# Kernel optimization log

Measured on AMD Instinct MI355X. Metric: run time of the kernel, lower is better.

The kernel has to match this reference:

```python
import jax, jax.numpy as jnp
import numpy as np

B = 65536          # batch
E = 512            # embedding_dim
SL = 128           # speed_latent_dim
H = 256            # hidden_size
NB = 6             # num_branch
D = E + SL         # 640, branch input dim


def _linear_init(k, din, dout):
    bound = 1.0 / np.sqrt(din)
    kw, kb = jax.random.split(k)
    W = jax.random.uniform(kw, (din, dout), minval=-bound, maxval=bound, dtype=jnp.float32)
    b = jax.random.uniform(kb, (dout,), minval=-bound, maxval=bound, dtype=jnp.float32)
    return W, b


def setup_inputs() -> dict:
    key = jax.random.key(0)
    ks = jax.random.split(key, 10)
    embedding = jax.random.normal(ks[0], (B, E), dtype=jnp.float32)
    speed = jax.random.uniform(ks[1], (B, 1), dtype=jnp.float32)
    command = jax.random.randint(ks[2], (B,), 1, NB + 1)  # values in 1..6

    # speed_in: Linear(1,H) -> ReLU -> Linear(H,SL)
    si_W1, si_b1 = _linear_init(ks[3], 1, H)
    si_W2, si_b2 = _linear_init(ks[4], H, SL)

    # speed_out: Linear(D,H) -> ReLU -> Linear(H,H) -> ReLU -> Linear(H,1)
    so_W1, so_b1 = _linear_init(ks[5], D, H)
    so_W2, so_b2 = _linear_init(ks[6], H, H)
    so_W3, so_b3 = _linear_init(ks[7], H, 1)

    # NB branches, each Linear(D,H)->ReLU->Linear(H,H)->ReLU->Linear(H,3)->Sigmoid
    def mk_branch(k):
        k1, k2, k3 = jax.random.split(k, 3)
        W1, b1 = _linear_init(k1, D, H)
        W2, b2 = _linear_init(k2, H, H)
        W3, b3 = _linear_init(k3, H, 3)
        return W1, b1, W2, b2, W3, b3

    bW1, bb1, bW2, bb2, bW3, bb3 = jax.vmap(mk_branch)(jax.random.split(ks[8], NB))

    return {
        "embedding": embedding, "speed": speed, "command": command,
        "si_W1": si_W1, "si_b1": si_b1, "si_W2": si_W2, "si_b2": si_b2,
        "bW1": bW1, "bb1": bb1, "bW2": bW2, "bb2": bb2, "bW3": bW3, "bb3": bb3,
        "so_W1": so_W1, "so_b1": so_b1, "so_W2": so_W2, "so_b2": so_b2,
        "so_W3": so_W3, "so_b3": so_b3,
    }


def reference(embedding, speed, command,
              si_W1, si_b1, si_W2, si_b2,
              bW1, bb1, bW2, bb2, bW3, bb3,
              so_W1, so_b1, so_W2, so_b2, so_W3, so_b3):
    # speed_in MLP and concat
    s = jax.nn.relu(speed @ si_W1 + si_b1) @ si_W2 + si_b2          # [B, SL]
    emb = jnp.concatenate([embedding, s], axis=1)                    # [B, D]

    # all branches computed densely (as in the torch module), then one-hot mask
    h1 = jax.nn.relu(jnp.einsum('bd,ndh->nbh', emb, bW1) + bb1[:, None, :])   # [NB,B,H]
    h2 = jax.nn.relu(jnp.einsum('nbh,nhk->nbk', h1, bW2) + bb2[:, None, :])   # [NB,B,H]
    out = jax.nn.sigmoid(jnp.einsum('nbk,nko->nbo', h2, bW3) + bb3[:, None, :])  # [NB,B,3]

    mask = (jnp.arange(NB)[:, None] == (command - 1)[None, :]).astype(out.dtype)  # [NB,B]
    control_pred = jnp.sum(out * mask[:, :, None], axis=0)           # [B, 3]

    # speed prediction head
    sp = jax.nn.relu(emb @ so_W1 + so_b1)
    sp = jax.nn.relu(sp @ so_W2 + so_b2)
    speed_pred = sp @ so_W3 + so_b3                                  # [B, 1]

    return control_pred, speed_pred
```

## Files before the change

### kernel.cpp

```cpp
#include <hip/hip_runtime.h>
#include <cstdint>
#include <cstddef>

typedef _Float16 f16;
typedef f16 f16x8 __attribute__((ext_vector_type(8)));
typedef float f32x4 __attribute__((ext_vector_type(4)));

#define B_ROWS 65536
#define TILE_M 128
#define NT_BRANCH 518
#define NT_SPEED 512

constexpr size_t OFF_SF16   = 0;
constexpr size_t SZ_SF16    = (size_t)B_ROWS * 128 * 2;
constexpr size_t OFF_SIW2T  = OFF_SF16 + SZ_SF16;
constexpr size_t SZ_SIW2T   = (size_t)128 * 256 * 2;
constexpr size_t OFF_BW1T   = OFF_SIW2T + SZ_SIW2T;
constexpr size_t SZ_BW1T    = (size_t)6 * 256 * 640 * 2;
constexpr size_t OFF_BW2T   = OFF_BW1T + SZ_BW1T;
constexpr size_t SZ_BW2T    = (size_t)6 * 256 * 256 * 2;
constexpr size_t OFF_SOW1T  = OFF_BW2T + SZ_BW2T;
constexpr size_t SZ_SOW1T   = (size_t)256 * 640 * 2;
constexpr size_t OFF_SOW2T  = OFF_SOW1T + SZ_SOW1T;
constexpr size_t SZ_SOW2T   = (size_t)256 * 256 * 2;
constexpr size_t OFF_BW3T16 = OFF_SOW2T + SZ_SOW2T;
constexpr size_t SZ_BW3T16  = (size_t)6 * 16 * 256 * 2;
constexpr size_t OFF_SOW3T16= OFF_BW3T16 + SZ_BW3T16;
constexpr size_t SZ_SOW3T16 = (size_t)16 * 256 * 2;
constexpr size_t OFF_COUNTS = OFF_SOW3T16 + SZ_SOW3T16;
constexpr size_t OFF_CURSORS= OFF_COUNTS + 256;
constexpr size_t OFF_BINBASE= OFF_CURSORS + 256;
constexpr size_t OFF_TILECMD= OFF_BINBASE + 256;
constexpr size_t OFF_PERM   = OFF_TILECMD + 4352;
constexpr size_t WS_NEEDED  = OFF_PERM + (size_t)NT_BRANCH * TILE_M * 4;

#define MFMA16(a, b, c) __builtin_amdgcn_mfma_f32_16x16x32_f16(a, b, c, 0, 0, 0)
#define BARSYNC() asm volatile("s_waitcnt lgkmcnt(0)\n\ts_barrier" ::: "memory")

__global__ void prep_kernel(const float* __restrict__ siW2,
                            const float* __restrict__ bW1,
                            const float* __restrict__ bW2,
                            const float* __restrict__ soW1,
                            const float* __restrict__ soW2,
                            const float* __restrict__ bW3,
                            const float* __restrict__ soW3,
                            f16* __restrict__ siW2T, f16* __restrict__ bW1T,
                            f16* __restrict__ bW2T, f16* __restrict__ soW1T,
                            f16* __restrict__ soW2T,
                            f16* __restrict__ bW3T16, f16* __restrict__ soW3T16,
                            int* __restrict__ counts, int* __restrict__ cursors,
                            int* __restrict__ perm)
{
    const int bx = blockIdx.x;
    const int tx = threadIdx.x, ty = threadIdx.y;
    const int tid = ty * 32 + tx;
    if (bx >= 1601) {
        const int ib = bx - 1601;
        const int idx = ib * 256 + tid;
        if (idx < NT_BRANCH * TILE_M) perm[idx] = -1;
        if (ib == 0 && tid < 6) { counts[tid] = 0; cursors[tid] = 0; }
        return;
    }
    if (bx == 1600) {
        for (int i = tid; i < 6 * 16 * 256; i += 256) {
            const int c = i >> 12, rem = i & 4095, n = rem >> 8, k = rem & 255;
            bW3T16[i] = (n < 3) ? (f16)bW3[((size_t)c * 256 + k) * 3 + n] : (f16)0;
        }
        for (int i = tid; i < 16 * 256; i += 256) {
            const int n = i >> 8, k = i & 255;
            soW3T16[i] = (n == 0) ? (f16)soW3[k] : (f16)0;
        }
        return;
    }
    const float* in; f16* out; int R, C, lb;
    if (bx < 960)       { int m = bx / 160;        lb = bx - m * 160;       in = bW1 + (size_t)m * 640 * 256; out = bW1T + (size_t)m * 640 * 256; R = 640; C = 256; }
    else if (bx < 1344) { int m = (bx - 960) / 64; lb = (bx - 960) - m * 64; in = bW2 + (size_t)m * 256 * 256; out = bW2T + (size_t)m * 256 * 256; R = 256; C = 256; }
    else if (bx < 1504) { lb = bx - 1344; in = soW1; out = soW1T; R = 640; C = 256; }
    else if (bx < 1568) { lb = bx - 1504; in = soW2; out = soW2T; R = 256; C = 256; }
    else                { lb = bx - 1568; in = siW2; out = siW2T; R = 256; C = 128; }
    const int txt = C >> 5;
    const int c0 = (lb % txt) << 5;
    const int r0 = (lb / txt) << 5;
    __shared__ float tile[32][33];
    #pragma unroll
    for (int i = 0; i < 4; ++i)
        tile[tx][ty + 8 * i] = in[(size_t)(r0 + ty + 8 * i) * C + c0 + tx];
    __syncthreads();
    #pragma unroll
    for (int i = 0; i < 4; ++i)
        out[(size_t)(c0 + ty + 8 * i) * R + r0 + tx] = (f16)tile[ty + 8 * i][tx];
}

__global__ __launch_bounds__(256) void speedin_kernel(
    const float* __restrict__ speed,
    const float* __restrict__ siW1, const float* __restrict__ sib1,
    const f16* __restrict__ siW2T, const float* __restrict__ sib2,
    const int* __restrict__ cmd,
    f16* __restrict__ sF16, int* __restrict__ counts)
{
    __shared__ f16 H[64 * 264];
    __shared__ float spd[64];
    __shared__ int h[6];
    const int tid = threadIdx.x;
    const int rb = blockIdx.x * 64;
    if (tid < 6) h[tid] = 0;
    __syncthreads();
    if (tid < 64) {
        spd[tid] = speed[rb + tid];
        atomicAdd(&h[cmd[rb + tid] - 1], 1);
    }
    __syncthreads();
    if (tid < 6 && h[tid] > 0) atomicAdd(&counts[tid], h[tid]);
    {
        const float w1 = siW1[tid], b1v = sib1[tid];
        #pragma unroll 4
        for (int r = 0; r < 64; ++r) {
            float hv = spd[r] * w1 + b1v;
            H[r * 264 + tid] = (f16)(hv > 0.f ? hv : 0.f);
        }
    }
    __syncthreads();
    const int w = tid >> 6, lane = tid & 63, lq = lane >> 4, l16 = lane & 15;
    const int nb = w * 32;
    f32x4 acc[4][2];
    #pragma unroll
    for (int mt = 0; mt < 4; ++mt)
        #pragma unroll
        for (int nt = 0; nt < 2; ++nt)
            acc[mt][nt] = (f32x4){0.f, 0.f, 0.f, 0.f};
    for (int ks = 0; ks < 8; ++ks) {
        const int koff = ks * 32 + lq * 8;
        f16x8 af[4], bf[2];
        #pragma unroll
        for (int mt = 0; mt < 4; ++mt)
            af[mt] = *(const f16x8*)(&H[(mt * 16 + l16) * 264 + koff]);
        #pragma unroll
        for (int nt = 0; nt < 2; ++nt)
            bf[nt] = *(const f16x8*)(siW2T + (size_t)(nb + nt * 16 + l16) * 256 + koff);
        #pragma unroll
        for (int mt = 0; mt < 4; ++mt)
            #pragma unroll
            for (int nt = 0; nt < 2; ++nt)
                acc[mt][nt] = MFMA16(af[mt], bf[nt], acc[mt][nt]);
    }
    #pragma unroll
    for (int mt = 0; mt < 4; ++mt)
        #pragma unroll
        for (int nt = 0; nt < 2; ++nt) {
            const int n = nb + nt * 16 + l16;
            const float bv = sib2[n];
            #pragma unroll
            for (int r2 = 0; r2 < 4; ++r2) {
                const int m = mt * 16 + lq * 4 + r2;
                sF16[(size_t)(rb + m) * 128 + n] = (f16)(acc[mt][nt][r2] + bv);
            }
        }
}

__global__ void plan_kernel(const int* __restrict__ counts,
                            int* __restrict__ binBase, int* __restrict__ tile_cmd) {
    __shared__ int tbase[7];
    if (threadIdx.x == 0) {
        int base = 0, tb = 0;
        for (int c = 0; c < 6; ++c) {
            binBase[c] = base;
            tbase[c] = tb;
            const int nt = (counts[c] + TILE_M - 1) >> 7;
            tb += nt;
            base += nt << 7;
        }
        tbase[6] = tb;
    }
    __syncthreads();
    for (int t = threadIdx.x; t < NT_BRANCH; t += 256) {
        int c = -1;
        #pragma unroll
        for (int j = 0; j < 6; ++j)
            if (t >= tbase[j] && t < tbase[j + 1]) c = j;
        tile_cmd[t] = c;
    }
}

__global__ void place_kernel(const int* __restrict__ cmd,
                             const int* __restrict__ binBase,
                             int* __restrict__ cursors, int* __restrict__ perm) {
    __shared__ int lcnt[6], lbase[6];
    const int tid = threadIdx.x;
    if (tid < 6) lcnt[tid] = 0;
    __syncthreads();
    const int i = blockIdx.x * 256 + tid;
    const int c = cmd[i] - 1;
    const int myr = atomicAdd(&lcnt[c], 1);
    __syncthreads();
    if (tid < 6) lbase[tid] = atomicAdd(&cursors[tid], lcnt[tid]);
    __syncthreads();
    perm[binBase[c] + lbase[c] + myr] = i;
}

__device__ __forceinline__ void stage_load2(const float* __restrict__ srcF,
                                            const f16* __restrict__ srcH,
                                            int kc, int p, f16x8* v) {
    if (kc < 8) {
        const float* s = srcF + kc * 64 + p * 16;
        const float4 f0 = ((const float4*)s)[0];
        const float4 f1 = ((const float4*)s)[1];
        const float4 f2 = ((const float4*)s)[2];
        const float4 f3 = ((const float4*)s)[3];
        f16x8 a, b;
        a[0] = (f16)f0.x; a[1] = (f16)f0.y; a[2] = (f16)f0.z; a[3] = (f16)f0.w;
        a[4] = (f16)f1.x; a[5] = (f16)f1.y; a[6] = (f16)f1.z; a[7] = (f16)f1.w;
        b[0] = (f16)f2.x; b[1] = (f16)f2.y; b[2] = (f16)f2.z; b[3] = (f16)f2.w;
        b[4] = (f16)f3.x; b[5] = (f16)f3.y; b[6] = (f16)f3.z; b[7] = (f16)f3.w;
        v[0] = a; v[1] = b;
    } else {
        const f16* s = srcH + (kc - 8) * 64 + p * 16;
        v[0] = ((const f16x8*)s)[0];
        v[1] = ((const f16x8*)s)[1];
    }
}

__global__ __launch_bounds__(512, 3) void heads_kernel(
    const float* __restrict__ emb,
    const f16* __restrict__ sF16,
    const int* __restrict__ perm, const int* __restrict__ tile_cmd,
    const f16* __restrict__ bW1T, const f16* __restrict__ bW2T,
    const f16* __restrict__ bW3T16,
    const float* __restrict__ bb1, const float* __restrict__ bb2,
    const float* __restrict__ bb3,
    const f16* __restrict__ soW1T, const f16* __restrict__ soW2T,
    const f16* __restrict__ soW3T16,
    const float* __restrict__ sob1, const float* __restrict__ sob2,
    const float* __restrict__ sob3,
    float* __restrict__ out)
{
    __shared__ f16 smem[33792];
    __shared__ int rowIdx[TILE_M];
    const int bx = blockIdx.x;
    const int tid = threadIdx.x;
    const bool is_speed = (bx >= NT_BRANCH);
    const f16 *W1T, *W2T, *W3T;
    const float *bias1, *bias2, *bias3;
    if (is_speed) {
        const int t = bx - NT_BRANCH;
        if (tid < TILE_M) rowIdx[tid] = t * TILE_M + tid;
        W1T = soW1T; W2T = soW2T; W3T = soW3T16;
        bias1 = sob1; bias2 = sob2; bias3 = sob3;
    } else {
        const int c = tile_cmd[bx];
        if (c < 0) return;
        if (tid < TILE_M) rowIdx[tid] = perm[bx * TILE_M + tid];
        W1T = bW1T + (size_t)c * 256 * 640;
        W2T = bW2T + (size_t)c * 256 * 256;
        W3T = bW3T16 + (size_t)c * 16 * 256;
        bias1 = bb1 + c * 256; bias2 = bb2 + c * 256; bias3 = bb3 + c * 3;
    }
    __syncthreads();

    const int r = tid >> 2, p = tid & 3;
    int growS = rowIdx[r]; if (growS < 0) growS = 0;
    const float* srcF = emb + (size_t)growS * 512;
    const f16*   srcH = sF16 + (size_t)growS * 128;
    const int pOff = r * 72 + p * 16;

    const int w = tid >> 6, lane = tid & 63, lq = lane >> 4, l16 = lane & 15;
    const int nb = w * 32;
    const f16* brow0 = W1T + (size_t)(nb + l16) * 640;
    const f16* brow1 = W1T + (size_t)(nb + 16 + l16) * 640;

    f32x4 acc[8][2];
    #pragma unroll
    for (int mt = 0; mt < 8; ++mt)
        #pragma unroll
        for (int nt = 0; nt < 2; ++nt)
            acc[mt][nt] = (f32x4){0.f, 0.f, 0.f, 0.f};

    f16x8 sreg[3][2];
    #pragma unroll
    for (int j = 0; j < 3; ++j)
        stage_load2(srcF, srcH, j, p, sreg[j]);
    f16x8 Bb[2][2];
    #pragma unroll
    for (int ks = 0; ks < 2; ++ks) {
        Bb[ks][0] = *(const f16x8*)(brow0 + ks * 32 + lq * 8);
        Bb[ks][1] = *(const f16x8*)(brow1 + ks * 32 + lq * 8);
    }
    *(f16x8*)(smem + pOff) = sreg[0][0];
    *(f16x8*)(smem + pOff + 8) = sreg[0][1];
    BARSYNC();

    #pragma unroll
    for (int kc = 0; kc < 10; ++kc) {
        const f16* cur = smem + (kc & 1) * 9216;
        if (kc < 9) {
            f16* dst = smem + ((kc + 1) & 1) * 9216 + pOff;
            *(f16x8*)(dst)     = sreg[(kc + 1) % 3][0];
            *(f16x8*)(dst + 8) = sreg[(kc + 1) % 3][1];
        }
        if (kc < 7)
            stage_load2(srcF, srcH, kc + 3, p, sreg[kc % 3]);
        f16x8 Bn[2][2];
        if (kc < 9) {
            #pragma unroll
            for (int ks = 0; ks < 2; ++ks) {
                Bn[ks][0] = *(const f16x8*)(brow0 + (kc + 1) * 64 + ks * 32 + lq * 8);
                Bn[ks][1] = *(const f16x8*)(brow1 + (kc + 1) * 64 + ks * 32 + lq * 8);
            }
        }
        #pragma unroll
        for (int ks = 0; ks < 2; ++ks)
            #pragma unroll
            for (int mh = 0; mh < 2; ++mh) {
                f16x8 a[4];
                #pragma unroll
                for (int mt = 0; mt < 4; ++mt)
                    a[mt] = *(const f16x8*)(cur + ((mh * 4 + mt) * 16 + l16) * 72 + ks * 32 + lq * 8);
                #pragma unroll
                for (int mt = 0; mt < 4; ++mt) {
                    acc[mh * 4 + mt][0] = MFMA16(a[mt], Bb[ks][0], acc[mh * 4 + mt][0]);
                    acc[mh * 4 + mt][1] = MFMA16(a[mt], Bb[ks][1], acc[mh * 4 + mt][1]);
                }
            }
        if (kc < 9) {
            #pragma unroll
            for (int ks = 0; ks < 2; ++ks)
                #pragma unroll
                for (int nt = 0; nt < 2; ++nt)
                    Bb[ks][nt] = Bn[ks][nt];
        }
        BARSYNC();
    }

    const f16* brow2[2];
    #pragma unroll
    for (int nt = 0; nt < 2; ++nt)
        brow2[nt] = W2T + (size_t)(nb + nt * 16 + l16) * 256;
    f16x8 Bd[2][2];
    #pragma unroll
    for (int nt = 0; nt < 2; ++nt)
        Bd[0][nt] = *(const f16x8*)(brow2[nt] + lq * 8);

    #pragma unroll
    for (int mt = 0; mt < 8; ++mt)
        #pragma unroll
        for (int nt = 0; nt < 2; ++nt) {
            const int n = nb + nt * 16 + l16;
            const float bv = bias1[n];
            #pragma unroll
            for (int r2 = 0; r2 < 4; ++r2) {
                const int m = mt * 16 + lq * 4 + r2;
                const float v = acc[mt][nt][r2] + bv;
                smem[m * 264 + n] = (f16)(v > 0.f ? v : 0.f);
            }
            acc[mt][nt] = (f32x4){0.f, 0.f, 0.f, 0.f};
        }
    BARSYNC();

    #pragma unroll
    for (int ks = 0; ks < 8; ++ks) {
        if (ks < 7) {
            #pragma unroll
            for (int nt = 0; nt < 2; ++nt)
                Bd[(ks + 1) & 1][nt] = *(const f16x8*)(brow2[nt] + (ks + 1) * 32 + lq * 8);
        }
        #pragma unroll
        for (int mh = 0; mh < 2; ++mh) {
            f16x8 a[4];
            #pragma unroll
            for (int mt = 0; mt < 4; ++mt)
                a[mt] = *(const f16x8*)(&smem[((mh * 4 + mt) * 16 + l16) * 264 + ks * 32 + lq * 8]);
            #pragma unroll
            for (int mt = 0; mt < 4; ++mt) {
                acc[mh * 4 + mt][0] = MFMA16(a[mt], Bd[ks & 1][0], acc[mh * 4 + mt][0]);
                acc[mh * 4 + mt][1] = MFMA16(a[mt], Bd[ks & 1][1], acc[mh * 4 + mt][1]);
            }
        }
    }
    BARSYNC();
    #pragma unroll
    for (int mt = 0; mt < 8; ++mt)
        #pragma unroll
        for (int nt = 0; nt < 2; ++nt) {
            const int n = nb + nt * 16 + l16;
            const float bv = bias2[n];
            #pragma unroll
            for (int r2 = 0; r2 < 4; ++r2) {
                const int m = mt * 16 + lq * 4 + r2;
                const float v = acc[mt][nt][r2] + bv;
                smem[m * 264 + n] = (f16)(v > 0.f ? v : 0.f);
            }
        }
    BARSYNC();
    {
        f32x4 acc3 = (f32x4){0.f, 0.f, 0.f, 0.f};
        const f16* w3row = W3T + (size_t)l16 * 256;
        #pragma unroll
        for (int ks = 0; ks < 8; ++ks) {
            const int koff = ks * 32 + lq * 8;
            const f16x8 af = *(const f16x8*)(&smem[(w * 16 + l16) * 264 + koff]);
            const f16x8 bf = *(const f16x8*)(w3row + koff);
            acc3 = MFMA16(af, bf, acc3);
        }
        const int orow = w * 16 + lq * 4;
        if (!is_speed) {
            if (l16 < 3) {
                const float b3 = bias3[l16];
                #pragma unroll
                for (int r2 = 0; r2 < 4; ++r2) {
                    const int g = rowIdx[orow + r2];
                    if (g >= 0)
                        out[(size_t)g * 3 + l16] = 1.f / (1.f + __expf(-(acc3[r2] + b3)));
                }
            }
        } else {
            if (l16 == 0) {
                const float b3 = bias3[0];
                #pragma unroll
                for (int r2 = 0; r2 < 4; ++r2) {
                    const int g = rowIdx[orow + r2];
                    if (g >= 0)
                        out[(size_t)3 * B_ROWS + g] = acc3[r2] + b3;
                }
            }
        }
    }
}

extern "C" void kernel_launch(void* const* d_in, const int* in_sizes, int n_in,
                              void* d_out, int out_size, void* d_ws, size_t ws_size,
                              hipStream_t stream) {
    (void)in_sizes; (void)n_in; (void)out_size; (void)ws_size;
    const float* embedding = (const float*)d_in[0];
    const float* speed     = (const float*)d_in[1];
    const int*   command   = (const int*)d_in[2];
    const float* si_W1 = (const float*)d_in[3];
    const float* si_b1 = (const float*)d_in[4];
    const float* si_W2 = (const float*)d_in[5];
    const float* si_b2 = (const float*)d_in[6];
    const float* bW1   = (const float*)d_in[7];
    const float* bb1   = (const float*)d_in[8];
    const float* bW2   = (const float*)d_in[9];
    const float* bb2   = (const float*)d_in[10];
    const float* bW3   = (const float*)d_in[11];
    const float* bb3   = (const float*)d_in[12];
    const float* so_W1 = (const float*)d_in[13];
    const float* so_b1 = (const float*)d_in[14];
    const float* so_W2 = (const float*)d_in[15];
    const float* so_b2 = (const float*)d_in[16];
    const float* so_W3 = (const float*)d_in[17];
    const float* so_b3 = (const float*)d_in[18];
    float* out = (float*)d_out;

    char* ws = (char*)d_ws;
    f16* sF16   = (f16*)(ws + OFF_SF16);
    f16* siW2T  = (f16*)(ws + OFF_SIW2T);
    f16* bW1T   = (f16*)(ws + OFF_BW1T);
    f16* bW2T   = (f16*)(ws + OFF_BW2T);
    f16* soW1T  = (f16*)(ws + OFF_SOW1T);
    f16* soW2T  = (f16*)(ws + OFF_SOW2T);
    f16* bW3T16 = (f16*)(ws + OFF_BW3T16);
    f16* soW3T16= (f16*)(ws + OFF_SOW3T16);
    int* counts = (int*)(ws + OFF_COUNTS);
    int* cursors= (int*)(ws + OFF_CURSORS);
    int* binBase= (int*)(ws + OFF_BINBASE);
    int* tile_cmd = (int*)(ws + OFF_TILECMD);
    int* perm   = (int*)(ws + OFF_PERM);

    prep_kernel<<<1860, dim3(32, 8), 0, stream>>>(
        si_W2, bW1, bW2, so_W1, so_W2, bW3, so_W3,
        siW2T, bW1T, bW2T, soW1T, soW2T, bW3T16, soW3T16,
        counts, cursors, perm);
    speedin_kernel<<<1024, 256, 0, stream>>>(
        speed, si_W1, si_b1, siW2T, si_b2, command, sF16, counts);
    plan_kernel<<<1, 256, 0, stream>>>(counts, binBase, tile_cmd);
    place_kernel<<<256, 256, 0, stream>>>(command, binBase, cursors, perm);
    heads_kernel<<<NT_BRANCH + NT_SPEED, 512, 0, stream>>>(
        embedding, sF16, perm, tile_cmd,
        bW1T, bW2T, bW3T16, bb1, bb2, bb3,
        soW1T, soW2T, soW3T16, so_b1, so_b2, so_b3, out);
}
```

Before: 366.0 us.

## Pre-convert embedding to fp16 concatenated activation buffer in speedin kernel

The speedin kernel now converts the fp32 embedding to fp16 and writes it, together with the speed latent, into a single row-major [B,640] fp16 buffer. The heads kernel reads its A operand only from this buffer with uniform 16-byte loads and a 4-deep register prefetch, instead of loading and converting fp32 rows. Each embedding row is gathered by one branch tile and one speed tile, so the conversion cost and fp32 read traffic in the heads kernel drop. The cost is an extra 80MB fp16 write plus re-read through a larger workspace.

```diff
diff --git a/kernel.cpp b/kernel.cpp
--- a/kernel.cpp
+++ b/kernel.cpp
@@ -11,9 +11,9 @@
 #define NT_BRANCH 518
 #define NT_SPEED 512
 
-constexpr size_t OFF_SF16   = 0;
-constexpr size_t SZ_SF16    = (size_t)B_ROWS * 128 * 2;
-constexpr size_t OFF_SIW2T  = OFF_SF16 + SZ_SF16;
+constexpr size_t OFF_AF16   = 0;
+constexpr size_t SZ_AF16    = (size_t)B_ROWS * 640 * 2;
+constexpr size_t OFF_SIW2T  = OFF_AF16 + SZ_AF16;
 constexpr size_t SZ_SIW2T   = (size_t)128 * 256 * 2;
 constexpr size_t OFF_BW1T   = OFF_SIW2T + SZ_SIW2T;
 constexpr size_t SZ_BW1T    = (size_t)6 * 256 * 640 * 2;
@@ -92,11 +92,12 @@
 }
 
 __global__ __launch_bounds__(256) void speedin_kernel(
+    const float* __restrict__ emb,
     const float* __restrict__ speed,
     const float* __restrict__ siW1, const float* __restrict__ sib1,
     const f16* __restrict__ siW2T, const float* __restrict__ sib2,
     const int* __restrict__ cmd,
-    f16* __restrict__ sF16, int* __restrict__ counts)
+    f16* __restrict__ AF16, int* __restrict__ counts)
 {
     __shared__ f16 H[64 * 264];
     __shared__ float spd[64];
@@ -112,6 +113,20 @@
     __syncthreads();
     if (tid < 6 && h[tid] > 0) atomicAdd(&counts[tid], h[tid]);
     {
+        const int rr = tid >> 2, pp = tid & 3;
+        const float* src = emb + (size_t)(rb + rr) * 512 + pp * 128;
+        f16* dst = AF16 + (size_t)(rb + rr) * 640 + pp * 128;
+        #pragma unroll 4
+        for (int i = 0; i < 16; ++i) {
+            const float4 f0 = ((const float4*)src)[2 * i];
+            const float4 f1 = ((const float4*)src)[2 * i + 1];
+            f16x8 v;
+            v[0] = (f16)f0.x; v[1] = (f16)f0.y; v[2] = (f16)f0.z; v[3] = (f16)f0.w;
+            v[4] = (f16)f1.x; v[5] = (f16)f1.y; v[6] = (f16)f1.z; v[7] = (f16)f1.w;
+            *(f16x8*)(dst + i * 8) = v;
+        }
+    }
+    {
         const float w1 = siW1[tid], b1v = sib1[tid];
         #pragma unroll 4
         for (int r = 0; r < 64; ++r) {
@@ -152,7 +167,7 @@
             #pragma unroll
             for (int r2 = 0; r2 < 4; ++r2) {
                 const int m = mt * 16 + lq * 4 + r2;
-                sF16[(size_t)(rb + m) * 128 + n] = (f16)(acc[mt][nt][r2] + bv);
+                AF16[(size_t)(rb + m) * 640 + 512 + n] = (f16)(acc[mt][nt][r2] + bv);
             }
         }
 }
@@ -197,31 +212,8 @@
     perm[binBase[c] + lbase[c] + myr] = i;
 }
 
-__device__ __forceinline__ void stage_load2(const float* __restrict__ srcF,
-                                            const f16* __restrict__ srcH,
-                                            int kc, int p, f16x8* v) {
-    if (kc < 8) {
-        const float* s = srcF + kc * 64 + p * 16;
-        const float4 f0 = ((const float4*)s)[0];
-        const float4 f1 = ((const float4*)s)[1];
-        const float4 f2 = ((const float4*)s)[2];
-        const float4 f3 = ((const float4*)s)[3];
-        f16x8 a, b;
-        a[0] = (f16)f0.x; a[1] = (f16)f0.y; a[2] = (f16)f0.z; a[3] = (f16)f0.w;
-        a[4] = (f16)f1.x; a[5] = (f16)f1.y; a[6] = (f16)f1.z; a[7] = (f16)f1.w;
-        b[0] = (f16)f2.x; b[1] = (f16)f2.y; b[2] = (f16)f2.z; b[3] = (f16)f2.w;
-        b[4] = (f16)f3.x; b[5] = (f16)f3.y; b[6] = (f16)f3.z; b[7] = (f16)f3.w;
-        v[0] = a; v[1] = b;
-    } else {
-        const f16* s = srcH + (kc - 8) * 64 + p * 16;
-        v[0] = ((const f16x8*)s)[0];
-        v[1] = ((const f16x8*)s)[1];
-    }
-}
-
 __global__ __launch_bounds__(512, 3) void heads_kernel(
-    const float* __restrict__ emb,
-    const f16* __restrict__ sF16,
+    const f16* __restrict__ AF16,
     const int* __restrict__ perm, const int* __restrict__ tile_cmd,
     const f16* __restrict__ bW1T, const f16* __restrict__ bW2T,
     const f16* __restrict__ bW3T16,
@@ -258,8 +250,7 @@
 
     const int r = tid >> 2, p = tid & 3;
     int growS = rowIdx[r]; if (growS < 0) growS = 0;
-    const float* srcF = emb + (size_t)growS * 512;
-    const f16*   srcH = sF16 + (size_t)growS * 128;
+    const f16* srcA = AF16 + (size_t)growS * 640 + p * 16;
     const int pOff = r * 72 + p * 16;
 
     const int w = tid >> 6, lane = tid & 63, lq = lane >> 4, l16 = lane & 15;
@@ -274,10 +265,12 @@
         for (int nt = 0; nt < 2; ++nt)
             acc[mt][nt] = (f32x4){0.f, 0.f, 0.f, 0.f};
 
-    f16x8 sreg[3][2];
-    #pragma unroll
-    for (int j = 0; j < 3; ++j)
-        stage_load2(srcF, srcH, j, p, sreg[j]);
+    f16x8 sreg[4][2];
+    #pragma unroll
+    for (int j = 0; j < 4; ++j) {
+        sreg[j][0] = ((const f16x8*)(srcA + j * 64))[0];
+        sreg[j][1] = ((const f16x8*)(srcA + j * 64))[1];
+    }
     f16x8 Bb[2][2];
     #pragma unroll
     for (int ks = 0; ks < 2; ++ks) {
@@ -293,11 +286,13 @@
         const f16* cur = smem + (kc & 1) * 9216;
         if (kc < 9) {
             f16* dst = smem + ((kc + 1) & 1) * 9216 + pOff;
-            *(f16x8*)(dst)     = sreg[(kc + 1) % 3][0];
-            *(f16x8*)(dst + 8) = sreg[(kc + 1) % 3][1];
-        }
-        if (kc < 7)
-            stage_load2(srcF, srcH, kc + 3, p, sreg[kc % 3]);
+            *(f16x8*)(dst)     = sreg[(kc + 1) & 3][0];
+            *(f16x8*)(dst + 8) = sreg[(kc + 1) & 3][1];
+        }
+        if (kc < 6) {
+            sreg[kc & 3][0] = ((const f16x8*)(srcA + (kc + 4) * 64))[0];
+            sreg[kc & 3][1] = ((const f16x8*)(srcA + (kc + 4) * 64))[1];
+        }
         f16x8 Bn[2][2];
         if (kc < 9) {
             #pragma unroll
@@ -451,7 +446,7 @@
     float* out = (float*)d_out;
 
     char* ws = (char*)d_ws;
-    f16* sF16   = (f16*)(ws + OFF_SF16);
+    f16* AF16   = (f16*)(ws + OFF_AF16);
     f16* siW2T  = (f16*)(ws + OFF_SIW2T);
     f16* bW1T   = (f16*)(ws + OFF_BW1T);
     f16* bW2T   = (f16*)(ws + OFF_BW2T);
@@ -470,11 +465,11 @@
         siW2T, bW1T, bW2T, soW1T, soW2T, bW3T16, soW3T16,
         counts, cursors, perm);
     speedin_kernel<<<1024, 256, 0, stream>>>(
-        speed, si_W1, si_b1, siW2T, si_b2, command, sF16, counts);
+        embedding, speed, si_W1, si_b1, siW2T, si_b2, command, AF16, counts);
     plan_kernel<<<1, 256, 0, stream>>>(counts, binBase, tile_cmd);
     place_kernel<<<256, 256, 0, stream>>>(command, binBase, cursors, perm);
     heads_kernel<<<NT_BRANCH + NT_SPEED, 512, 0, stream>>>(
-        embedding, sF16, perm, tile_cmd,
+        AF16, perm, tile_cmd,
         bW1T, bW2T, bW3T16, bb1, bb2, bb3,
         soW1T, soW2T, soW3T16, so_b1, so_b2, so_b3, out);
 }
```

Result: slower. 392.0 us (+7.1%).
